# Kernel optimization log

Hardware: AMD Instinct MI355X
Metric: run time of the kernel (lower is better)

## Reference

```python
import jax, jax.numpy as jnp
import numpy as np

# dims (see shape_source)
E, L, PE = 128, 16, 33          # events, latent dim, time-vector dim (1+16+16)
F, W, HOP, C = 256, 512, 256, 257  # gen frames, window, hop, rfft coeffs
H, NL, GP = 512, 4, 128         # hidden, n_layers, generator pos channels
N = F * HOP                     # segment samples = 65536
TOTAL = 1048576                 # model total_samples
F2 = 2 * F                      # scheduling frames over padded (2*N) window


def _time_vec(t):
    # time_vector(): rows = [t, sin(t*f), cos(t*f)] -> (33, n)
    t = t.reshape(1, -1)
    fr = jnp.linspace(1.0, TOTAL / 2, PE // 2)[:, None]
    return jnp.concatenate([t, jnp.sin(t * fr), jnp.cos(t * fr)], axis=0)


def setup_inputs() -> dict:
    key = jax.random.key(0)
    ks = jax.random.split(key, 12)
    std = 0.05
    # learned per-event time vectors (pre-masked to the segment window)
    t_ev = jax.random.uniform(ks[0], (E,), minval=-1.0, maxval=1.0)
    times = _time_vec(t_ev).T  # (E, 33)
    # frame positional encodings over the doubled window [early_frame, end_frame]
    s0 = 0.25
    s1 = s0 + (2 * N) / TOTAL
    tpos = jnp.linspace(s0 * 2 * np.pi, s1 * 2 * np.pi, F2)
    pos_encoding = _time_vec(tpos).T[None]  # (1, F2, 33)
    events = jax.random.uniform(ks[1], (E, L), minval=-1.0, maxval=1.0)
    # EventGenerator's decayed random pos-encoding buffer
    pe = jax.random.uniform(ks[2], (1, F, GP), minval=-1.0, maxval=1.0)
    decay = jnp.linspace(1.0, 0.0, F)
    pwr = jax.random.uniform(ks[3], (GP,), minval=10.0, maxval=100.0)
    gen_pos = pe * decay[None, :, None] ** pwr[None, None, :]  # (1, F, GP)
    # uniform(-1,1) noise used by materialize_phase dithering
    dither_noise = jax.random.uniform(ks[4], (1, F, C), minval=-1.0, maxval=1.0)
    w_ee = jax.random.normal(ks[5], (H, L)) * std
    b_ee = jnp.zeros((H,))
    w_ep = jax.random.normal(ks[6], (H, GP)) * std
    b_ep = jnp.zeros((H,))
    net_w = jax.random.normal(ks[7], (NL, H, H)) * std
    net_b = jnp.zeros((NL, H))
    w_mag = jax.random.normal(ks[8], (C, H)) * std
    b_mag = jnp.zeros((C,))
    w_dith = jax.random.normal(ks[9], (C, H)) * std
    b_dith = jnp.zeros((C,))
    return dict(events=events, times=times, pos_encoding=pos_encoding,
                gen_pos=gen_pos, dither_noise=dither_noise,
                w_ee=w_ee, b_ee=b_ee, w_ep=w_ep, b_ep=b_ep,
                net_w=net_w, net_b=net_b, w_mag=w_mag, b_mag=b_mag,
                w_dith=w_dith, b_dith=b_dith)


def reference(events, times, pos_encoding, gen_pos, dither_noise,
              w_ee, b_ee, w_ep, b_ep, net_w, net_b,
              w_mag, b_mag, w_dith, b_dith):
    # ---- EventGenerator ----
    e = events @ w_ee.T + b_ee                  # (E, H)
    p = gen_pos @ w_ep.T + b_ep                 # (1, F, H)
    x = e[:, None, :] + p[0][None]              # (E, F, H)
    for i in range(net_w.shape[0]):
        x = x + jax.nn.selu(x @ net_w[i].T + net_b[i])
    m = jnp.abs(x @ w_mag.T + b_mag)            # (E, F, C)
    d = x @ w_dith.T + b_dith                   # (E, F, C)
    gd = jnp.linspace(0.0, np.pi, C).astype(x.dtype)[None, None, :]
    phase = jnp.cumsum(gd + d * gd * dither_noise, axis=1)  # accumulate over frames
    spec = m * jnp.exp(1j * phase)
    windowed = jnp.fft.irfft(spec, n=W, axis=-1, norm='ortho')  # (E, F, W)
    # overlap-add with hann window, half-lapped (hop = W//2)
    win = (0.5 - 0.5 * jnp.cos(2 * np.pi * jnp.arange(W) / W)).astype(x.dtype)
    windowed = windowed * win
    even = windowed[:, 0::2].reshape(E, -1)     # occupies [0, N)
    odd = windowed[:, 1::2].reshape(E, -1)      # occupies [HOP, N+HOP)
    buf = jnp.zeros((E, N + HOP), dtype=x.dtype)
    buf = buf.at[:, :N].add(even).at[:, HOP:].add(odd)
    samples = buf[:, :N]                        # (E, N)
    # pad with zeros (Model.forward) -> length 2N
    padded = jnp.concatenate([samples, jnp.zeros_like(samples)], axis=-1)
    # ---- schedule_events ----
    sim = jnp.einsum('ed,fd->ef', times, pos_encoding[0])  # (E, F2)
    # sparse_softmax(normalize=True): one-hot of argmax with value 1
    sched = jax.nn.one_hot(jnp.argmax(sim, axis=-1), F2, dtype=padded.dtype)
    # upsample_with_holes: stride HOP, zeros between frames -> (E, 2N)
    sched_up = jnp.pad(sched[..., None], ((0, 0), (0, 0), (0, HOP - 1))).reshape(E, 2 * N)
    # fft_convolve (circular)
    conv = jnp.fft.irfft(jnp.fft.rfft(padded, axis=-1) * jnp.fft.rfft(sched_up, axis=-1),
                         n=2 * N, axis=-1)      # (E, 2N)
    scheduled = jnp.sum(conv, axis=0)[None, None, :]  # (1, 1, 2N)
    return scheduled[:, :, N:]                  # (1, 1, N)
```

## Files before the change

### kernel.cpp

```cpp
#include <hip/hip_runtime.h>
#include <math.h>

#define E_N   128
#define L_N   16
#define PE_N  33
#define F_N   256
#define W_N   512
#define HOP_N 256
#define C_N   257
#define H_N   512
#define GP_N  128
#define F2_N  512
#define NSAMP (F_N*HOP_N)
#define M_ROWS (E_N*F_N)
#define KLD   544
#define MDLD  544
#define WMD_N 640
#define KC    16

#define BM 128
#define BN 128

typedef float f32x4 __attribute__((ext_vector_type(4)));
typedef short s16x8 __attribute__((ext_vector_type(8)));

__device__ __forceinline__ float selu_f(float x){
    const float alpha = 1.6732632423543772f;
    const float scale = 1.0507009873554805f;
    return scale * (x > 0.f ? x : alpha * expm1f(x));
}
__device__ __forceinline__ unsigned short f2bf(float x){
    unsigned u = __float_as_uint(x);
    return (unsigned short)((u + 0x7fffu + ((u >> 16) & 1u)) >> 16);
}
__device__ __forceinline__ float bf2f(unsigned short h){
    return __uint_as_float((unsigned)h << 16);
}
__device__ __forceinline__ void split2(float x, unsigned short* h, unsigned short* l){
    unsigned short hh = f2bf(x);
    *h = hh;
    *l = f2bf(x - bf2f(hh));
}

__global__ __launch_bounds__(256,2) void k_mfma_gemm(
    const unsigned short* __restrict__ Ah, const unsigned short* __restrict__ Al, int lda,
    const unsigned short* __restrict__ Bh, const unsigned short* __restrict__ Bl, int ldb,
    const float* __restrict__ bias,
    unsigned short* __restrict__ Oh, unsigned short* __restrict__ Ol,
    float* __restrict__ Cf, int ldc,
    int K, int mode, int Ncols)
{
    __shared__ unsigned short sm[16384];
    const int tid  = threadIdx.x;
    const int w    = tid >> 6;
    const int lane = tid & 63;

    const int gx = gridDim.x;
    const int nwg = gx * gridDim.y;
    const int h = blockIdx.y * gx + blockIdx.x;
    const int t = (h & 7) * (nwg >> 3) + (h >> 3);
    const int row0 = (t / gx) * BM;
    const int col0 = (t - (t / gx) * gx) * BN;

    const int wr = w >> 1, wc = w & 1;

    f32x4 acc[4][4] = {};

    for (int k0 = 0; k0 < K; k0 += 32) {
        #pragma unroll
        for (int i = 0; i < 8; ++i) {
            int ci = i*256 + w*64 + lane;
            int c  = ci & 511;
            int kg = c >> 7, r = c & 127;
            const unsigned short* gp;
            if      (i < 2) gp = Ah + (size_t)(row0 + r)*lda + (k0 + kg*8);
            else if (i < 4) gp = Al + (size_t)(row0 + r)*lda + (k0 + kg*8);
            else if (i < 6) gp = Bh + (size_t)(col0 + r)*ldb + (k0 + kg*8);
            else            gp = Bl + (size_t)(col0 + r)*ldb + (k0 + kg*8);
            __builtin_amdgcn_global_load_lds(
                (const __attribute__((address_space(1))) void*)gp,
                (__attribute__((address_space(3))) void*)(&sm[ci*8]),
                16, 0, 0);
        }
        __syncthreads();

        const int kg = lane >> 4, lr = lane & 15;
        s16x8 ah[4], al[4], bh[4], bl[4];
        #pragma unroll
        for (int m = 0; m < 4; ++m) {
            int off = (kg*128 + wr*64 + m*16 + lr)*8;
            ah[m] = *(const s16x8*)&sm[off];
            al[m] = *(const s16x8*)&sm[4096 + off];
        }
        #pragma unroll
        for (int n = 0; n < 4; ++n) {
            int off = (kg*128 + wc*64 + n*16 + lr)*8;
            bh[n] = *(const s16x8*)&sm[8192 + off];
            bl[n] = *(const s16x8*)&sm[12288 + off];
        }
        #pragma unroll
        for (int m = 0; m < 4; ++m)
            #pragma unroll
            for (int n = 0; n < 4; ++n) {
                acc[m][n] = __builtin_amdgcn_mfma_f32_16x16x32_bf16(ah[m], bh[n], acc[m][n], 0,0,0);
                acc[m][n] = __builtin_amdgcn_mfma_f32_16x16x32_bf16(ah[m], bl[n], acc[m][n], 0,0,0);
                acc[m][n] = __builtin_amdgcn_mfma_f32_16x16x32_bf16(al[m], bh[n], acc[m][n], 0,0,0);
            }
        __syncthreads();
    }

    const int lr = lane & 15, q = lane >> 4;
    if (mode == 0) {
        #pragma unroll
        for (int n = 0; n < 4; ++n) {
            int col = col0 + wc*64 + n*16 + lr;
            float bv = bias[col];
            #pragma unroll
            for (int m = 0; m < 4; ++m) {
                int rb = row0 + wr*64 + m*16 + q*4;
                #pragma unroll
                for (int g = 0; g < 4; ++g) {
                    size_t idx = (size_t)(rb + g)*lda + col;
                    float resid = bf2f(Ah[idx]) + bf2f(Al[idx]);
                    float o = resid + selu_f(acc[m][n][g] + bv);
                    unsigned short hh = f2bf(o);
                    Oh[idx] = hh;
                    Ol[idx] = f2bf(o - bf2f(hh));
                }
            }
        }
    } else if (mode == 1) {
        #pragma unroll
        for (int n = 0; n < 4; ++n) {
            int col = col0 + wc*64 + n*16 + lr;
            if (col < Ncols) {
                float bv = bias[col];
                bool isev = !(col & 1);
                #pragma unroll
                for (int m = 0; m < 4; ++m) {
                    int rb = row0 + wr*64 + m*16 + q*4;
                    #pragma unroll
                    for (int g = 0; g < 4; ++g) {
                        float v = acc[m][n][g] + bv;
                        if (isev) v = fabsf(v);
                        Cf[(size_t)(rb + g)*ldc + col] = v;
                    }
                }
            }
        }
    } else {
        #pragma unroll
        for (int n = 0; n < 4; ++n) {
            int col = col0 + wc*64 + n*16 + lr;
            #pragma unroll
            for (int m = 0; m < 4; ++m) {
                int rb = row0 + wr*64 + m*16 + q*4;
                #pragma unroll
                for (int g = 0; g < 4; ++g)
                    Cf[(size_t)(rb + g)*ldc + col] = acc[m][n][g];
            }
        }
    }
}


__global__ void k_eproj(const float* __restrict__ ev, const float* __restrict__ w,
                        const float* __restrict__ b, float* __restrict__ e_buf){
    int idx = blockIdx.x*256 + threadIdx.x;
    int ei = idx >> 9, h = idx & 511;
    float acc = b[h];
    #pragma unroll
    for (int l = 0; l < L_N; ++l) acc = fmaf(ev[ei*L_N+l], w[h*L_N+l], acc);
    e_buf[idx] = acc;
}

__global__ void k_pproj(const float* __restrict__ gp, const float* __restrict__ w,
                        const float* __restrict__ b, float* __restrict__ p_buf){
    int idx = blockIdx.x*256 + threadIdx.x;
    int f = idx >> 9, h = idx & 511;
    float acc = b[h];
    #pragma unroll 8
    for (int g = 0; g < GP_N; ++g) acc = fmaf(gp[f*GP_N+g], w[h*GP_N+g], acc);
    p_buf[idx] = acc;
}

__global__ void k_xinit_bf(const float4* __restrict__ e_buf, const float4* __restrict__ p_buf,
                           unsigned short* __restrict__ xh, unsigned short* __restrict__ xl){
    int idx = blockIdx.x*256 + threadIdx.x;
    int h4 = idx & 127;
    int r  = idx >> 7;
    int ei = r >> 8, f = r & 255;
    float4 a = e_buf[ei*128 + h4];
    float4 b = p_buf[f*128 + h4];
    float o[4] = {a.x+b.x, a.y+b.y, a.z+b.z, a.w+b.w};
    unsigned short hh[4], ll[4];
    #pragma unroll
    for (int j = 0; j < 4; ++j) split2(o[j], &hh[j], &ll[j]);
    size_t base = (size_t)r*H_N + h4*4;
    *(ushort4*)&xh[base] = make_ushort4(hh[0], hh[1], hh[2], hh[3]);
    *(ushort4*)&xl[base] = make_ushort4(ll[0], ll[1], ll[2], ll[3]);
}

__global__ void k_split4(const float4* __restrict__ src, unsigned short* __restrict__ oh,
                         unsigned short* __restrict__ ol, int n4){
    int i = blockIdx.x*256 + threadIdx.x;
    if (i >= n4) return;
    float4 v = src[i];
    float o[4] = {v.x, v.y, v.z, v.w};
    unsigned short hh[4], ll[4];
    #pragma unroll
    for (int j = 0; j < 4; ++j) split2(o[j], &hh[j], &ll[j]);
    *(ushort4*)&oh[(size_t)i*4] = make_ushort4(hh[0], hh[1], hh[2], hh[3]);
    *(ushort4*)&ol[(size_t)i*4] = make_ushort4(ll[0], ll[1], ll[2], ll[3]);
}

__global__ void k_wmd(const float* __restrict__ wm, const float* __restrict__ wd,
                      const float* __restrict__ bm, const float* __restrict__ bd,
                      unsigned short* __restrict__ wh, unsigned short* __restrict__ wl,
                      float* __restrict__ bmd){
    int idx = blockIdx.x*256 + threadIdx.x;
    if (idx >= WMD_N*H_N) return;
    int m = idx >> 9, h = idx & 511;
    float v = 0.f;
    if (m < 2*C_N) v = (m & 1) ? wd[(m>>1)*H_N + h] : wm[(m>>1)*H_N + h];
    split2(v, &wh[idx], &wl[idx]);
    if (idx < WMD_N) {
        float b = 0.f;
        if (idx < 2*C_N) b = (idx & 1) ? bd[idx>>1] : bm[idx>>1];
        bmd[idx] = b;
    }
}

__global__ void k_basis_bf(unsigned short* __restrict__ bh, unsigned short* __restrict__ bl){
    int idx = blockIdx.x*256 + threadIdx.x;
    if (idx >= F2_N*KLD) return;
    int n = idx / KLD, kr = idx - n*KLD;
    float val = 0.f;
    if (kr < 2*C_N) {
        int k = kr >> 1;
        float wk = (k==0 || k==C_N-1) ? 1.f : 2.f;
        int j = (k*n) & 511;
        float ang = (float)((double)j * 0.01227184630308513);
        float s, c;
        sincosf(ang, &s, &c);
        float wang = (float)((double)n * 0.01227184630308513);
        float win = 0.5f - 0.5f*cosf(wang);
        const float rs = 0.04419417382415922f;
        val = ((kr & 1) ? -s : c) * wk * win * rs;
    }
    split2(val, &bh[idx], &bl[idx]);
}

__global__ void k_sim(const float* __restrict__ times, const float* __restrict__ pos,
                      int* __restrict__ pidx){
    __shared__ float sv[512];
    __shared__ int   si[512];
    int e = blockIdx.x, f = threadIdx.x;
    float acc = 0.f;
    #pragma unroll
    for (int d = 0; d < PE_N; ++d) acc = fmaf(times[e*PE_N+d], pos[f*PE_N+d], acc);
    sv[f] = acc; si[f] = f;
    __syncthreads();
    for (int off = 256; off > 0; off >>= 1) {
        if (f < off) {
            float v2 = sv[f+off]; int i2 = si[f+off];
            if (v2 > sv[f] || (v2 == sv[f] && i2 < si[f])) { sv[f]=v2; si[f]=i2; }
        }
        __syncthreads();
    }
    if (f == 0) pidx[e] = si[0];
}

__global__ void k_phase(const float* __restrict__ md, const float* __restrict__ noise,
                        unsigned short* __restrict__ ch, unsigned short* __restrict__ cl){
    int k0 = blockIdx.x * KC;
    int e  = blockIdx.y;
    int f  = threadIdx.x;
    size_t row = (size_t)(e*F_N + f);

    float mdv[2*KC];
    const float4* mp = (const float4*)(md + row*MDLD + 2*k0);
    #pragma unroll
    for (int i = 0; i < (2*KC)/4; ++i) *(float4*)&mdv[4*i] = mp[i];

    const int lane = f & 63, wv = f >> 6;
    __shared__ float wsum[KC][4];
    float ph[KC];
    #pragma unroll
    for (int kk = 0; kk < KC; ++kk) {
        int k = k0 + kk;
        float p = 0.f;
        if (k < C_N) {
            float d  = mdv[2*kk+1];
            float nz = noise[(size_t)f*C_N + k];
            float gdk = (float)(3.141592653589793/256.0) * (float)k;
            p = gdk + d*gdk*nz;
        }
        #pragma unroll
        for (int off = 1; off < 64; off <<= 1) {
            float t = __shfl_up(p, off);
            if (lane >= off) p += t;
        }
        if (lane == 63) wsum[kk][wv] = p;
        ph[kk] = p;
    }
    __syncthreads();

    unsigned short oh[2*KC], ol[2*KC];
    #pragma unroll
    for (int kk = 0; kk < KC; ++kk) {
        int k = k0 + kk;
        if (k < C_N) {
            float p = ph[kk];
            #pragma unroll
            for (int i = 0; i < 3; ++i) if (i < wv) p += wsum[kk][i];
            float sv, cv;
            sincosf(p, &sv, &cv);
            float m = mdv[2*kk];
            split2(m*cv, &oh[2*kk],   &ol[2*kk]);
            split2(m*sv, &oh[2*kk+1], &ol[2*kk+1]);
        } else {
            oh[2*kk] = 0; oh[2*kk+1] = 0;
            ol[2*kk] = 0; ol[2*kk+1] = 0;
        }
    }
    size_t o = row*KLD + 2*k0;
    #pragma unroll
    for (int i = 0; i < 4; ++i) {
        ((uint4*)(ch + o))[i] = ((const uint4*)oh)[i];
        ((uint4*)(cl + o))[i] = ((const uint4*)ol)[i];
    }
}

__global__ void k_gather(const float* __restrict__ wnd, const int* __restrict__ pidx,
                         float* __restrict__ out){
    __shared__ int sp[E_N];
    int tid = threadIdx.x;
    if (tid < E_N) sp[tid] = pidx[tid]*HOP_N;
    __syncthreads();
    int t = blockIdx.x*256 + tid;
    float acc = 0.f;
    #pragma unroll 4
    for (int e = 0; e < E_N; ++e) {
        int s = t + NSAMP - sp[e];
        if ((unsigned)s < (unsigned)NSAMP) {
            int f1 = s >> 8, n1 = s & 255;
            const float* base = wnd + ((size_t)(e*F_N + f1) << 9);
            acc += base[n1];
            if (f1 > 0) acc += base[n1 + 256 - 512];
        }
    }
    out[t] = acc;
}

extern "C" void kernel_launch(void* const* d_in, const int* in_sizes, int n_in,
                              void* d_out, int out_size, void* d_ws, size_t ws_size,
                              hipStream_t stream) {
    const float* events  = (const float*)d_in[0];
    const float* times   = (const float*)d_in[1];
    const float* pos     = (const float*)d_in[2];
    const float* gen_pos = (const float*)d_in[3];
    const float* noise   = (const float*)d_in[4];
    const float* w_ee    = (const float*)d_in[5];
    const float* b_ee    = (const float*)d_in[6];
    const float* w_ep    = (const float*)d_in[7];
    const float* b_ep    = (const float*)d_in[8];
    const float* net_w   = (const float*)d_in[9];
    const float* net_b   = (const float*)d_in[10];
    const float* w_mag   = (const float*)d_in[11];
    const float* b_mag   = (const float*)d_in[12];
    const float* w_dith  = (const float*)d_in[13];
    const float* b_dith  = (const float*)d_in[14];
    float* out = (float*)d_out;

    char* ws8 = (char*)d_ws;
    unsigned short* xAh = (unsigned short*)(ws8);
    unsigned short* xAl = (unsigned short*)(ws8 + 33554432ull);
    unsigned short* xBh = (unsigned short*)(ws8 + 67108864ull);
    unsigned short* xBl = (unsigned short*)(ws8 + 100663296ull);
    float*          cs32= (float*)(ws8 + 67108864ull);
    unsigned short* csh = (unsigned short*)(ws8);
    unsigned short* csl = (unsigned short*)(ws8 + 138412032ull);
    float*          bufB= (float*)(ws8 + 67108864ull);
    char* sp = ws8 + 174063616ull;
    unsigned short* bash = (unsigned short*)sp;  sp += 557056;
    unsigned short* basl = (unsigned short*)sp;  sp += 557056;
    unsigned short* nwh  = (unsigned short*)sp;  sp += 2097152;
    unsigned short* nwl  = (unsigned short*)sp;  sp += 2097152;
    unsigned short* wmdh = (unsigned short*)sp;  sp += 655360;
    unsigned short* wmdl = (unsigned short*)sp;  sp += 655360;
    float* bmd   = (float*)sp;                   sp += 4096;
    float* e_buf = (float*)sp;                   sp += 262144;
    float* p_buf = (float*)sp;                   sp += 524288;
    int*   pidx  = (int*)sp;

    k_basis_bf<<<(F2_N*KLD + 255)/256, 256, 0, stream>>>(bash, basl);
    k_sim<<<E_N, 512, 0, stream>>>(times, pos, pidx);
    k_split4<<<1024, 256, 0, stream>>>((const float4*)net_w, nwh, nwl, 4*H_N*H_N/4);
    k_wmd<<<(WMD_N*H_N + 255)/256, 256, 0, stream>>>(w_mag, w_dith, b_mag, b_dith, wmdh, wmdl, bmd);
    k_eproj<<<(E_N*H_N)/256, 256, 0, stream>>>(events, w_ee, b_ee, e_buf);
    k_pproj<<<(F_N*H_N)/256, 256, 0, stream>>>(gen_pos, w_ep, b_ep, p_buf);
    k_xinit_bf<<<(M_ROWS*(H_N/4))/256, 256, 0, stream>>>(
        (const float4*)e_buf, (const float4*)p_buf, xAh, xAl);

    unsigned short *ih = xAh, *il = xAl, *oh = xBh, *ol = xBl;
    for (int i = 0; i < 4; ++i) {
        k_mfma_gemm<<<dim3(H_N/BN, M_ROWS/BM), 256, 0, stream>>>(
            ih, il, H_N, nwh + (size_t)i*H_N*H_N, nwl + (size_t)i*H_N*H_N, H_N,
            net_b + (size_t)i*H_N, oh, ol, nullptr, 0, H_N, 0, H_N);
        unsigned short* t;
        t = ih; ih = oh; oh = t;
        t = il; il = ol; ol = t;
    }
    k_mfma_gemm<<<dim3(WMD_N/BN, M_ROWS/BM), 256, 0, stream>>>(
        ih, il, H_N, wmdh, wmdl, H_N, bmd, nullptr, nullptr, cs32, MDLD, H_N, 1, 2*C_N);

    k_phase<<<dim3(17, E_N), 256, 0, stream>>>(cs32, noise, csh, csl);

    k_mfma_gemm<<<dim3(F2_N/BN, M_ROWS/BM), 256, 0, stream>>>(
        csh, csl, KLD, bash, basl, KLD, nullptr, nullptr, nullptr, bufB, W_N, KLD, 3, F2_N);

    k_gather<<<NSAMP/256, 256, 0, stream>>>(bufB, pidx, out);
}
```

Baseline: 793.4 us.

## Double-buffer LDS tiles in MFMA GEMM to overlap global loads with compute

The GEMM kernel now uses two LDS buffers and prefetches the next K-tile through global_load_lds while the current tile feeds the MFMA instructions, so load latency can overlap with compute. The launch bounds occupancy hint also goes from 2 to 4 waves per SIMD. In exchange, LDS use per block doubles to 64KB, which may limit how many blocks fit per CU, and the higher occupancy hint may force register spills given the 64 accumulator floats per thread. Correctness depends on the tail sync keeping the prefetch from overwriting a buffer still being read.

```diff
diff --git a/kernel.cpp b/kernel.cpp
--- a/kernel.cpp
+++ b/kernel.cpp
@@ -42,7 +42,7 @@
     *l = f2bf(x - bf2f(hh));
 }
 
-__global__ __launch_bounds__(256,2) void k_mfma_gemm(
+__global__ __launch_bounds__(256,4) void k_mfma_gemm(
     const unsigned short* __restrict__ Ah, const unsigned short* __restrict__ Al, int lda,
     const unsigned short* __restrict__ Bh, const unsigned short* __restrict__ Bl, int ldb,
     const float* __restrict__ bias,
@@ -50,7 +50,7 @@
     float* __restrict__ Cf, int ldc,
     int K, int mode, int Ncols)
 {
-    __shared__ unsigned short sm[16384];
+    __shared__ unsigned short sm[2][16384];
     const int tid  = threadIdx.x;
     const int w    = tid >> 6;
     const int lane = tid & 63;
@@ -58,45 +58,68 @@
     const int gx = gridDim.x;
     const int nwg = gx * gridDim.y;
     const int h = blockIdx.y * gx + blockIdx.x;
-    const int t = (h & 7) * (nwg >> 3) + (h >> 3);
-    const int row0 = (t / gx) * BM;
-    const int col0 = (t - (t / gx) * gx) * BN;
+    const int t0 = (h & 7) * (nwg >> 3) + (h >> 3);
+    const int row0 = (t0 / gx) * BM;
+    const int col0 = (t0 - (t0 / gx) * gx) * BN;
 
     const int wr = w >> 1, wc = w & 1;
 
     f32x4 acc[4][4] = {};
 
-    for (int k0 = 0; k0 < K; k0 += 32) {
-        #pragma unroll
-        for (int i = 0; i < 8; ++i) {
-            int ci = i*256 + w*64 + lane;
-            int c  = ci & 511;
-            int kg = c >> 7, r = c & 127;
-            const unsigned short* gp;
-            if      (i < 2) gp = Ah + (size_t)(row0 + r)*lda + (k0 + kg*8);
-            else if (i < 4) gp = Al + (size_t)(row0 + r)*lda + (k0 + kg*8);
-            else if (i < 6) gp = Bh + (size_t)(col0 + r)*ldb + (k0 + kg*8);
-            else            gp = Bl + (size_t)(col0 + r)*ldb + (k0 + kg*8);
-            __builtin_amdgcn_global_load_lds(
-                (const __attribute__((address_space(1))) void*)gp,
-                (__attribute__((address_space(3))) void*)(&sm[ci*8]),
-                16, 0, 0);
-        }
-        __syncthreads();
-
-        const int kg = lane >> 4, lr = lane & 15;
+    int ci_[8], kg_[8], r_[8];
+    #pragma unroll
+    for (int i = 0; i < 8; ++i) {
+        int ci = i*256 + w*64 + lane;
+        int c  = ci & 511;
+        ci_[i] = ci; kg_[i] = c >> 7; r_[i] = c & 127;
+    }
+
+    #pragma unroll
+    for (int i = 0; i < 8; ++i) {
+        const unsigned short* gp;
+        if      (i < 2) gp = Ah + (size_t)(row0 + r_[i])*lda + kg_[i]*8;
+        else if (i < 4) gp = Al + (size_t)(row0 + r_[i])*lda + kg_[i]*8;
+        else if (i < 6) gp = Bh + (size_t)(col0 + r_[i])*ldb + kg_[i]*8;
+        else            gp = Bl + (size_t)(col0 + r_[i])*ldb + kg_[i]*8;
+        __builtin_amdgcn_global_load_lds(
+            (const __attribute__((address_space(1))) void*)gp,
+            (__attribute__((address_space(3))) void*)(&sm[0][ci_[i]*8]),
+            16, 0, 0);
+    }
+    __syncthreads();
+
+    const int nt = K >> 5;
+    const int kgl = lane >> 4, lr0 = lane & 15;
+    for (int t = 0; t < nt; ++t) {
+        const int cur = t & 1;
+        if (t + 1 < nt) {
+            const int k0 = (t + 1) << 5;
+            #pragma unroll
+            for (int i = 0; i < 8; ++i) {
+                const unsigned short* gp;
+                if      (i < 2) gp = Ah + (size_t)(row0 + r_[i])*lda + (k0 + kg_[i]*8);
+                else if (i < 4) gp = Al + (size_t)(row0 + r_[i])*lda + (k0 + kg_[i]*8);
+                else if (i < 6) gp = Bh + (size_t)(col0 + r_[i])*ldb + (k0 + kg_[i]*8);
+                else            gp = Bl + (size_t)(col0 + r_[i])*ldb + (k0 + kg_[i]*8);
+                __builtin_amdgcn_global_load_lds(
+                    (const __attribute__((address_space(1))) void*)gp,
+                    (__attribute__((address_space(3))) void*)(&sm[cur^1][ci_[i]*8]),
+                    16, 0, 0);
+            }
+        }
+
         s16x8 ah[4], al[4], bh[4], bl[4];
         #pragma unroll
         for (int m = 0; m < 4; ++m) {
-            int off = (kg*128 + wr*64 + m*16 + lr)*8;
-            ah[m] = *(const s16x8*)&sm[off];
-            al[m] = *(const s16x8*)&sm[4096 + off];
+            int off = (kgl*128 + wr*64 + m*16 + lr0)*8;
+            ah[m] = *(const s16x8*)&sm[cur][off];
+            al[m] = *(const s16x8*)&sm[cur][4096 + off];
         }
         #pragma unroll
         for (int n = 0; n < 4; ++n) {
-            int off = (kg*128 + wc*64 + n*16 + lr)*8;
-            bh[n] = *(const s16x8*)&sm[8192 + off];
-            bl[n] = *(const s16x8*)&sm[12288 + off];
+            int off = (kgl*128 + wc*64 + n*16 + lr0)*8;
+            bh[n] = *(const s16x8*)&sm[cur][8192 + off];
+            bl[n] = *(const s16x8*)&sm[cur][12288 + off];
         }
         #pragma unroll
         for (int m = 0; m < 4; ++m)
```

Result: no change. 778.1 us (-1.9%).
